# Kernel tuning notes

Measured on AMD Instinct MI355X. Metric: run time of the kernel, lower is better.

Reference implementation:

```python
import jax, jax.numpy as jnp
import numpy as np

B, T, F, H, O = 128, 4096, 80, 64, 8  # batch, seq_len, input_size, hidden_size, output_size


def setup_inputs() -> dict:
    key = jax.random.key(0)
    ks = jax.random.split(key, 12)
    s = 1.0 / np.sqrt(H)  # torch LSTM/Linear init scale

    def u(k, shape):
        return jax.random.uniform(k, shape, jnp.float32, -s, s)

    return {
        "x": jax.random.normal(ks[0], (B, T, F), jnp.float32),
        "lengths": jax.random.randint(ks[1], (B,), 1, T + 1),  # unused by forward, kept for signature fidelity
        "w_ih_f": u(ks[2], (4 * H, F)), "w_hh_f": u(ks[3], (4 * H, H)),
        "b_ih_f": u(ks[4], (4 * H,)), "b_hh_f": u(ks[5], (4 * H,)),
        "w_ih_b": u(ks[6], (4 * H, F)), "w_hh_b": u(ks[7], (4 * H, H)),
        "b_ih_b": u(ks[8], (4 * H,)), "b_hh_b": u(ks[9], (4 * H,)),
        "w_fc": u(ks[10], (O, 2 * H)), "b_fc": u(ks[11], (O,)),
    }


def _lstm_final_h(x, w_ih, w_hh, b_ih, b_hh):
    """Run a single-direction LSTM over x [B,T,F]; return final hidden state [B,H].
    PyTorch gate order: i, f, g, o."""
    pre = jnp.einsum('btf,gf->btg', x, w_ih) + (b_ih + b_hh)  # [B,T,4H], input projection hoisted out of scan
    h0 = jnp.zeros((x.shape[0], w_hh.shape[1]), x.dtype)

    def step(carry, g_t):
        h, c = carry
        gates = g_t + h @ w_hh.T  # [B,4H]
        i, f, g, o = jnp.split(gates, 4, axis=-1)
        c = jax.nn.sigmoid(f) * c + jax.nn.sigmoid(i) * jnp.tanh(g)
        h = jax.nn.sigmoid(o) * jnp.tanh(c)
        return (h, c), None

    (h, _), _ = jax.lax.scan(step, (h0, h0), jnp.swapaxes(pre, 0, 1))  # scan over time
    return h


def reference(x, lengths, w_ih_f, w_hh_f, b_ih_f, b_hh_f,
              w_ih_b, w_hh_b, b_ih_b, b_hh_b, w_fc, b_fc):
    # Bidirectional LSTM final hidden states: h[0]=forward final, h[1]=backward final.
    h_fwd = _lstm_final_h(x, w_ih_f, w_hh_f, b_ih_f, b_hh_f)
    h_bwd = _lstm_final_h(jnp.flip(x, axis=1), w_ih_b, w_hh_b, b_ih_b, b_hh_b)
    # permute (1,0,2) + reshape(B, 2H) of h [2,B,H] == concat along feature dim
    h = jnp.concatenate([h_fwd, h_bwd], axis=-1)  # [B, 2H]
    # nn.Dropout(0.5) in eval mode is identity (deterministic baseline)
    out = h @ w_fc.T + b_fc  # [B, O]
    return jnp.squeeze(out)
```

## Files before the change

kernel.cpp:

```cpp
#include <hip/hip_runtime.h>
#include <hip/hip_bf16.h>

#define TT 4096
#define FF 80
#define HH 64
#define NB 128
#define TB 256
#define CT 8
#define XPAD 104
#define LOG2E 1.44269504088896340736f

using short8  = __attribute__((ext_vector_type(8))) short;
using floatx4 = __attribute__((ext_vector_type(4))) float;

__device__ __forceinline__ float sigm(float x)  { return __builtin_amdgcn_rcpf(1.0f + __expf(-x)); }
__device__ __forceinline__ float tanh_f(float x){ return 1.0f - 2.0f * __builtin_amdgcn_rcpf(1.0f + __expf(2.0f * x)); }

__device__ __forceinline__ unsigned short f2bf(float f) {
    unsigned u = __builtin_bit_cast(unsigned, f);
    u += 0x7fffu + ((u >> 16) & 1u);
    return (unsigned short)(u >> 16);
}
__device__ __forceinline__ float bflo(unsigned u) { return __builtin_bit_cast(float, u << 16); }
__device__ __forceinline__ float bfhi(unsigned u) { return __builtin_bit_cast(float, u & 0xffff0000u); }
__device__ __forceinline__ unsigned packbf2(float a, float b) {
    return (unsigned)f2bf(a) | ((unsigned)f2bf(b) << 16);
}

__device__ __forceinline__ unsigned short cvt_bf16(float f) {
    unsigned r;
    asm("v_cvt_pk_bf16_f32 %0, %1, %2" : "=v"(r) : "v"(f), "v"(f));
    return (unsigned short)r;
}

__device__ __forceinline__ void bar_lgkm() {
    asm volatile("s_waitcnt lgkmcnt(0)" ::: "memory");
    __builtin_amdgcn_s_barrier();
}

__device__ __forceinline__ floatx4 mfma16(short8 a, short8 b, floatx4 c) {
    return __builtin_amdgcn_mfma_f32_16x16x32_bf16(a, b, c, 0, 0, 0);
}

__device__ __forceinline__ float sigm_s(float s) {
    return __builtin_amdgcn_rcpf(1.0f + __builtin_amdgcn_exp2f(-s));
}
__device__ __forceinline__ float tanh_s(float s) {
    return fmaf(-2.0f, __builtin_amdgcn_rcpf(1.0f + __builtin_amdgcn_exp2f(s + s)), 1.0f);
}

__global__ __launch_bounds__(256, 1)
void lstm_proj_mfma(const float* __restrict__ x,
                    const float* __restrict__ w_ih_f, const float* __restrict__ b_ih_f,
                    const float* __restrict__ b_hh_f,
                    const float* __restrict__ w_ih_b, const float* __restrict__ b_ih_b,
                    const float* __restrict__ b_hh_b,
                    unsigned short* __restrict__ pre)
{
    const int blk   = blockIdx.x;
    const int ttile = blk & 15;
    const int dgrp  = blk >> 4;
    const int dir   = dgrp >> 3;
    const int bgrp  = dgrp & 7;
    const int tid   = threadIdx.x;
    const int wv    = tid >> 6;
    const int l     = tid & 63;
    const int b16   = l & 15;
    const int g     = l >> 4;
    const int t0    = ttile * TB;

    const float* __restrict__ wih = dir ? w_ih_b : w_ih_f;
    const float* __restrict__ bi  = dir ? b_ih_b : b_ih_f;
    const float* __restrict__ bh  = dir ? b_hh_b : b_hh_f;

    short8 Bf[4][3];
    float  bias[4];
    #pragma unroll
    for (int tp = 0; tp < 4; ++tp) {
        const int n = 64 * wv + 16 * tp + b16;
        bias[tp] = (bi[n] + bh[n]) * LOG2E;
        #pragma unroll
        for (int kap = 0; kap < 3; ++kap) {
            const int f0 = 32 * kap + 8 * g;
            float f[8];
            if (f0 < FF) {
                const float4 v0 = *reinterpret_cast<const float4*>(wih + n * FF + f0);
                const float4 v1 = *reinterpret_cast<const float4*>(wih + n * FF + f0 + 4);
                f[0]=v0.x; f[1]=v0.y; f[2]=v0.z; f[3]=v0.w;
                f[4]=v1.x; f[5]=v1.y; f[6]=v1.z; f[7]=v1.w;
            } else {
                #pragma unroll
                for (int j = 0; j < 8; ++j) f[j] = 0.0f;
            }
            short8 s;
            #pragma unroll
            for (int j = 0; j < 8; ++j) s[j] = (short)f2bf(f[j] * LOG2E);
            Bf[tp][kap] = s;
        }
    }

    __shared__ __align__(16) unsigned short xa[2][CT][16][XPAD];
    for (int i = tid; i < 2 * CT * 16 * XPAD / 2; i += 256)
        reinterpret_cast<unsigned*>(&xa[0][0][0][0])[i] = 0u;
    __syncthreads();

    const int nph = TB / CT;

    {
        const int t0p = t0;
        const int te_base = dir ? (TT - CT - t0p) : t0p;
        float2 st[20];
        #pragma unroll
        for (int q = 0; q < 20; ++q) {
            const int i = q * 256 + tid;
            const int b = i / 320, r2 = i % 320;
            const int te_rel = r2 / 40, fq = r2 % 40;
            st[q] = *reinterpret_cast<const float2*>(
                x + ((size_t)(bgrp * 16 + b) * TT + te_base + te_rel) * FF + 2 * fq);
        }
        #pragma unroll
        for (int q = 0; q < 20; ++q) {
            const int i = q * 256 + tid;
            const int b = i / 320, r2 = i % 320;
            const int te_rel = r2 / 40, fq = r2 % 40;
            const int t_off = dir ? (CT - 1 - te_rel) : te_rel;
            *reinterpret_cast<unsigned*>(&xa[0][t_off][b][2 * fq]) = packbf2(st[q].x, st[q].y);
        }
    }
    __syncthreads();

    #pragma unroll 1
    for (int ph = 0; ph < nph; ++ph) {
        const int cur = ph & 1;
        const bool have = (ph + 1) < nph;

        float2 st[20];
        if (have) {
            const int t0p = t0 + (ph + 1) * CT;
            const int te_base = dir ? (TT - CT - t0p) : t0p;
            #pragma unroll
            for (int q = 0; q < 20; ++q) {
                const int i = q * 256 + tid;
                const int b = i / 320, r2 = i % 320;
                const int te_rel = r2 / 40, fq = r2 % 40;
                st[q] = *reinterpret_cast<const float2*>(
                    x + ((size_t)(bgrp * 16 + b) * TT + te_base + te_rel) * FF + 2 * fq);
            }
        }

        #pragma unroll
        for (int t_off = 0; t_off < CT; ++t_off) {
            short8 A[3];
            #pragma unroll
            for (int kap = 0; kap < 3; ++kap)
                A[kap] = *reinterpret_cast<const short8*>(&xa[cur][t_off][b16][32 * kap + 8 * g]);
            const int t = t0 + ph * CT + t_off;
            #pragma unroll
            for (int tp = 0; tp < 4; ++tp) {
                floatx4 acc = {bias[tp], bias[tp], bias[tp], bias[tp]};
                acc = mfma16(A[0], Bf[tp][0], acc);
                acc = mfma16(A[1], Bf[tp][1], acc);
                acc = mfma16(A[2], Bf[tp][2], acc);
                const int p = (16 * tp + b16) * 4 + wv;
                #pragma unroll
                for (int r = 0; r < 4; ++r) {
                    const int bb = dir * NB + bgrp * 16 + 4 * g + r;
                    pre[((size_t)bb * TT + t) * 256 + p] = f2bf(acc[r]);
                }
            }
        }

        if (have) {
            #pragma unroll
            for (int q = 0; q < 20; ++q) {
                const int i = q * 256 + tid;
                const int b = i / 320, r2 = i % 320;
                const int te_rel = r2 / 40, fq = r2 % 40;
                const int t_off = dir ? (CT - 1 - te_rel) : te_rel;
                *reinterpret_cast<unsigned*>(&xa[cur ^ 1][t_off][b][2 * fq]) = packbf2(st[q].x, st[q].y);
            }
        }
        bar_lgkm();
    }
}

__global__ __launch_bounds__(256, 1)
void lstm_scan_mfma4(const unsigned short* __restrict__ pre,
                     const float* __restrict__ w_hh_f, const float* __restrict__ w_hh_b,
                     float* __restrict__ h_out)
{
    const int chain = blockIdx.x;
    const int dir   = chain >> 7;
    const int tid   = threadIdx.x;
    const int wv    = tid >> 6;
    const int l     = tid & 63;
    const int b16   = l & 15;
    const int g4    = l >> 4;
    const bool actC = (g4 == 0);
    const int  u    = 16 * wv + b16;

    const float* __restrict__ whh = dir ? w_hh_b : w_hh_f;

    short8 Bf[4][2];
    #pragma unroll
    for (int gt = 0; gt < 4; ++gt) {
        const int n = gt * 64 + 16 * wv + b16;
        #pragma unroll
        for (int kap = 0; kap < 2; ++kap) {
            const float4 v0 = *reinterpret_cast<const float4*>(whh + n * HH + 32 * kap + 8 * g4);
            const float4 v1 = *reinterpret_cast<const float4*>(whh + n * HH + 32 * kap + 8 * g4 + 4);
            short8 s;
            s[0]=(short)f2bf(v0.x*LOG2E); s[1]=(short)f2bf(v0.y*LOG2E);
            s[2]=(short)f2bf(v0.z*LOG2E); s[3]=(short)f2bf(v0.w*LOG2E);
            s[4]=(short)f2bf(v1.x*LOG2E); s[5]=(short)f2bf(v1.y*LOG2E);
            s[6]=(short)f2bf(v1.z*LOG2E); s[7]=(short)f2bf(v1.w*LOG2E);
            Bf[gt][kap] = s;
        }
    }

    __shared__ __align__(16) unsigned short hls[192];
    if (tid < 96) reinterpret_cast<unsigned*>(hls)[tid] = 0u;

    const uint2* __restrict__ prow = reinterpret_cast<const uint2*>(
        pre + (size_t)chain * TT * 256 + u * 4);
    uint2 prr[4];
    if (actC) {
        #pragma unroll
        for (int d = 0; d < 4; ++d) prr[d] = prow[(size_t)d * 64];
    }

    float c = 0.0f, h = 0.0f;
    __syncthreads();

    const char* lb = reinterpret_cast<const char*>(hls);
    char* lw = reinterpret_cast<char*>(hls);

    #pragma unroll 1
    for (int t = 0; t < TT; t += 4) {
        #pragma unroll
        for (int d = 0; d < 4; ++d) {
            const int cur = d & 1;

            const int abase = (b16 == 0 ? 128 * cur : 256) + 16 * g4;
            const short8 A0 = *reinterpret_cast<const short8*>(lb + abase);
            const short8 A1 = *reinterpret_cast<const short8*>(lb + abase + 64);

            uint2 pc = prr[d];
            if (actC) prr[d] = prow[(size_t)((t + d + 4) & (TT - 1)) * 64];

            const floatx4 z = {0.f, 0.f, 0.f, 0.f};
            floatx4 ci0 = mfma16(A0, Bf[0][0], z), ci1 = mfma16(A1, Bf[0][1], z);
            floatx4 cf0 = mfma16(A0, Bf[1][0], z), cf1 = mfma16(A1, Bf[1][1], z);
            floatx4 cg0 = mfma16(A0, Bf[2][0], z), cg1 = mfma16(A1, Bf[2][1], z);
            floatx4 co0 = mfma16(A0, Bf[3][0], z), co1 = mfma16(A1, Bf[3][1], z);

            if (actC) {
                const float gi = bflo(pc.x) + (ci0[0] + ci1[0]);
                const float gf = bfhi(pc.x) + (cf0[0] + cf1[0]);
                const float gg = bflo(pc.y) + (cg0[0] + cg1[0]);
                const float go = bfhi(pc.y) + (co0[0] + co1[0]);
                c = fmaf(sigm_s(gf), c, sigm_s(gi) * tanh_s(gg));
                h = sigm_s(go) * tanh_s(c * LOG2E);
                *reinterpret_cast<unsigned short*>(lw + 128 * (cur ^ 1) + 2 * u) = cvt_bf16(h);
            }
            bar_lgkm();
        }
    }

    if (actC) h_out[(size_t)chain * HH + u] = h;
}

__global__ __launch_bounds__(256, 1)
void lstm_scan_fused_kernel(const float* __restrict__ x,
                            const float* __restrict__ w_ih_f, const float* __restrict__ w_hh_f,
                            const float* __restrict__ b_ih_f, const float* __restrict__ b_hh_f,
                            const float* __restrict__ w_ih_b, const float* __restrict__ w_hh_b,
                            const float* __restrict__ b_ih_b, const float* __restrict__ b_hh_b,
                            float* __restrict__ h_out)
{
    const int blk = blockIdx.x;
    const int dir = blk >> 7;
    const int bat = blk & 127;
    const int tid = threadIdx.x;
    const int wv  = tid >> 6;
    const int ln  = tid & 63;

    const float* __restrict__ w_ih = dir ? w_ih_b : w_ih_f;
    const float* __restrict__ w_hh = dir ? w_hh_b : w_hh_f;
    const float* __restrict__ b_ih = dir ? b_ih_b : b_ih_f;
    const float* __restrict__ b_hh = dir ? b_hh_b : b_hh_f;

    float wi[FF], wh[HH];
    #pragma unroll
    for (int f = 0; f < FF; ++f) wi[f] = w_ih[tid * FF + f];
    #pragma unroll
    for (int j = 0; j < HH; ++j) wh[j] = w_hh[tid * HH + j];
    const float bias = b_ih[tid] + b_hh[tid];

    __shared__ float xs[2][FF];
    __shared__ float hbuf[4][HH];
    __shared__ float gbuf[2][256];

    const float* __restrict__ xrow = x + (size_t)bat * (TT * FF);
    float c = 0.0f, hreg = 0.0f;
    hbuf[wv][ln] = 0.0f;

    float xA = 0.0f;
    if (tid < FF) {
        xs[0][tid] = xrow[(size_t)(dir ? (TT - 1) : 0) * FF + tid];
        xA         = xrow[(size_t)(dir ? (TT - 2) : 1) * FF + tid];
    }
    __syncthreads();

    #pragma unroll 1
    for (int t = 0; t < TT; ++t) {
        const int cur = t & 1, nxt = cur ^ 1;
        float a0 = 0.f, a1 = 0.f, a2 = 0.f, a3 = 0.f;
        const float4* xs4 = reinterpret_cast<const float4*>(xs[cur]);
        #pragma unroll
        for (int f = 0; f < FF / 4; ++f) {
            float4 v = xs4[f];
            a0 = fmaf(wi[4*f+0], v.x, a0);
            a1 = fmaf(wi[4*f+1], v.y, a1);
            a2 = fmaf(wi[4*f+2], v.z, a2);
            a3 = fmaf(wi[4*f+3], v.w, a3);
        }
        const float4* hb4 = reinterpret_cast<const float4*>(hbuf[wv]);
        #pragma unroll
        for (int j = 0; j < HH / 4; ++j) {
            float4 v = hb4[j];
            a0 = fmaf(wh[4*j+0], v.x, a0);
            a1 = fmaf(wh[4*j+1], v.y, a1);
            a2 = fmaf(wh[4*j+2], v.z, a2);
            a3 = fmaf(wh[4*j+3], v.w, a3);
        }
        gbuf[cur][tid] = ((a0 + a1) + (a2 + a3)) + bias;

        if (tid < FF) {
            if (t + 1 < TT) xs[nxt][tid] = xA;
            if (t + 2 < TT) xA = xrow[(size_t)(dir ? (TT - 3 - t) : (t + 2)) * FF + tid];
        }
        __syncthreads();

        const float gi = gbuf[cur][ln];
        const float gf = gbuf[cur][64 + ln];
        const float gg = gbuf[cur][128 + ln];
        const float go = gbuf[cur][192 + ln];
        c    = sigm(gf) * c + sigm(gi) * tanh_f(gg);
        hreg = sigm(go) * tanh_f(c);
        hbuf[wv][ln] = hreg;
    }

    if (tid < HH) h_out[(size_t)(dir * 128 + bat) * HH + tid] = hreg;
}

__global__ __launch_bounds__(64, 1)
void fc_kernel(const float* __restrict__ h_out,
               const float* __restrict__ w_fc,
               const float* __restrict__ b_fc,
               float* __restrict__ out)
{
    const int b = blockIdx.x;
    const int o = threadIdx.x;
    if (o < 8) {
        float acc = b_fc[o];
        #pragma unroll 4
        for (int j = 0; j < HH; ++j)
            acc = fmaf(h_out[(size_t)b * HH + j], w_fc[o * 128 + j], acc);
        #pragma unroll 4
        for (int j = 0; j < HH; ++j)
            acc = fmaf(h_out[(size_t)(NB + b) * HH + j], w_fc[o * 128 + 64 + j], acc);
        out[b * 8 + o] = acc;
    }
}

extern "C" void kernel_launch(void* const* d_in, const int* in_sizes, int n_in,
                              void* d_out, int out_size, void* d_ws, size_t ws_size,
                              hipStream_t stream) {
    const float* x      = (const float*)d_in[0];
    const float* w_ih_f = (const float*)d_in[2];
    const float* w_hh_f = (const float*)d_in[3];
    const float* b_ih_f = (const float*)d_in[4];
    const float* b_hh_f = (const float*)d_in[5];
    const float* w_ih_b = (const float*)d_in[6];
    const float* w_hh_b = (const float*)d_in[7];
    const float* b_ih_b = (const float*)d_in[8];
    const float* b_hh_b = (const float*)d_in[9];
    const float* w_fc   = (const float*)d_in[10];
    const float* b_fc   = (const float*)d_in[11];
    float* out = (float*)d_out;

    const size_t pre_bytes = (size_t)2 * NB * TT * 256 * 2;
    const size_t need      = pre_bytes + 64 * 1024;

    if (ws_size >= need) {
        unsigned short* pre = (unsigned short*)d_ws;
        float* h_out = (float*)((char*)d_ws + pre_bytes);
        lstm_proj_mfma<<<dim3(256), dim3(256), 0, stream>>>(
            x, w_ih_f, b_ih_f, b_hh_f, w_ih_b, b_ih_b, b_hh_b, pre);
        lstm_scan_mfma4<<<dim3(256), dim3(256), 0, stream>>>(
            pre, w_hh_f, w_hh_b, h_out);
        fc_kernel<<<dim3(128), dim3(64), 0, stream>>>(h_out, w_fc, b_fc, out);
    } else {
        float* h_out = (float*)d_ws;
        lstm_scan_fused_kernel<<<dim3(256), dim3(256), 0, stream>>>(
            x, w_ih_f, w_hh_f, b_ih_f, b_hh_f,
            w_ih_b, w_hh_b, b_ih_b, b_hh_b, h_out);
        fc_kernel<<<dim3(128), dim3(64), 0, stream>>>(h_out, w_fc, b_fc, out);
    }
}
```

Before: 1.431 ms.

## Interleave two LSTM chains per block in the recurrent scan kernel

```diff
diff --git a/kernel.cpp b/kernel.cpp
--- a/kernel.cpp
+++ b/kernel.cpp
@@ -9,6 +9,7 @@
 #define CT 8
 #define XPAD 104
 #define LOG2E 1.44269504088896340736f
+#define K2E   2.88539008177792681472f
 
 using short8  = __attribute__((ext_vector_type(8))) short;
 using floatx4 = __attribute__((ext_vector_type(4))) float;
@@ -185,19 +186,22 @@
 }
 
 __global__ __launch_bounds__(256, 1)
-void lstm_scan_mfma4(const unsigned short* __restrict__ pre,
-                     const float* __restrict__ w_hh_f, const float* __restrict__ w_hh_b,
-                     float* __restrict__ h_out)
+void lstm_scan_dual(const unsigned short* __restrict__ pre,
+                    const float* __restrict__ w_hh_f, const float* __restrict__ w_hh_b,
+                    float* __restrict__ h_out)
 {
-    const int chain = blockIdx.x;
-    const int dir   = chain >> 7;
-    const int tid   = threadIdx.x;
-    const int wv    = tid >> 6;
-    const int l     = tid & 63;
-    const int b16   = l & 15;
-    const int g4    = l >> 4;
-    const bool actC = (g4 == 0);
-    const int  u    = 16 * wv + b16;
+    const int blk    = blockIdx.x;
+    const int dir    = blk >> 6;
+    const int bat    = blk & 63;
+    const int chainA = dir * NB + bat;
+    const int chainB = chainA + 64;
+    const int tid    = threadIdx.x;
+    const int wv     = tid >> 6;
+    const int l      = tid & 63;
+    const int b16    = l & 15;
+    const int g4     = l >> 4;
+    const bool actC  = (g4 == 0);
+    const int  u     = 16 * wv + b16;
 
     const float* __restrict__ whh = dir ? w_hh_b : w_hh_f;
 
@@ -218,18 +222,24 @@
         }
     }
 
-    __shared__ __align__(16) unsigned short hls[192];
-    if (tid < 96) reinterpret_cast<unsigned*>(hls)[tid] = 0u;
-
-    const uint2* __restrict__ prow = reinterpret_cast<const uint2*>(
-        pre + (size_t)chain * TT * 256 + u * 4);
-    uint2 prr[4];
+    __shared__ __align__(16) unsigned short hls[320];
+    if (tid < 160) reinterpret_cast<unsigned*>(hls)[tid] = 0u;
+
+    const uint2* __restrict__ prowA = reinterpret_cast<const uint2*>(
+        pre + (size_t)chainA * TT * 256 + u * 4);
+    const uint2* __restrict__ prowB = reinterpret_cast<const uint2*>(
+        pre + (size_t)chainB * TT * 256 + u * 4);
+    uint2 prA[4] = {{0,0},{0,0},{0,0},{0,0}};
+    uint2 prB[4] = {{0,0},{0,0},{0,0},{0,0}};
+    const uint2 *pA0 = prowA + 4*64, *pA1 = prowA + 5*64, *pA2 = prowA + 6*64, *pA3 = prowA + 7*64;
+    const uint2 *pB0 = prowB + 4*64, *pB1 = prowB + 5*64, *pB2 = prowB + 6*64, *pB3 = prowB + 7*64;
     if (actC) {
-        #pragma unroll
-        for (int d = 0; d < 4; ++d) prr[d] = prow[(size_t)d * 64];
-    }
-
-    float c = 0.0f, h = 0.0f;
+        prA[0] = prowA[0*64]; prA[1] = prowA[1*64]; prA[2] = prowA[2*64]; prA[3] = prowA[3*64];
+        prB[0] = prowB[0*64]; prB[1] = prowB[1*64]; prB[2] = prowB[2*64]; prB[3] = prowB[3*64];
+    }
+
+    float c2A = 0.0f, hA = 0.0f;
+    float c2B = 0.0f, hB = 0.0f;
     __syncthreads();
 
     const char* lb = reinterpret_cast<const char*>(hls);
@@ -241,33 +251,67 @@
         for (int d = 0; d < 4; ++d) {
             const int cur = d & 1;
 
-            const int abase = (b16 == 0 ? 128 * cur : 256) + 16 * g4;
-            const short8 A0 = *reinterpret_cast<const short8*>(lb + abase);
-            const short8 A1 = *reinterpret_cast<const short8*>(lb + abase + 64);
-
-            uint2 pc = prr[d];
-            if (actC) prr[d] = prow[(size_t)((t + d + 4) & (TT - 1)) * 64];
+            const int abaseA = (b16 == 0 ? 128 * cur       : 256) + 16 * g4;
+            const int abaseB = (b16 == 0 ? 384 + 128 * cur : 256) + 16 * g4;
+            const short8 A0a = *reinterpret_cast<const short8*>(lb + abaseA);
+            const short8 A1a = *reinterpret_cast<const short8*>(lb + abaseA + 64);
+            const short8 A0b = *reinterpret_cast<const short8*>(lb + abaseB);
+            const short8 A1b = *reinterpret_cast<const short8*>(lb + abaseB + 64);
+
+            uint2 pcA = prA[d], pcB = prB[d];
+            if (actC) {
+                if (d == 0)      { prA[0] = *pA0; pA0 += 256; prB[0] = *pB0; pB0 += 256; }
+                else if (d == 1) { prA[1] = *pA1; pA1 += 256; prB[1] = *pB1; pB1 += 256; }
+                else if (d == 2) { prA[2] = *pA2; pA2 += 256; prB[2] = *pB2; pB2 += 256; }
+                else             { prA[3] = *pA3; pA3 += 256; prB[3] = *pB3; pB3 += 256; }
+            }
 
             const floatx4 z = {0.f, 0.f, 0.f, 0.f};
-            floatx4 ci0 = mfma16(A0, Bf[0][0], z), ci1 = mfma16(A1, Bf[0][1], z);
-            floatx4 cf0 = mfma16(A0, Bf[1][0], z), cf1 = mfma16(A1, Bf[1][1], z);
-            floatx4 cg0 = mfma16(A0, Bf[2][0], z), cg1 = mfma16(A1, Bf[2][1], z);
-            floatx4 co0 = mfma16(A0, Bf[3][0], z), co1 = mfma16(A1, Bf[3][1], z);
+            const floatx4 ciA = mfma16(A1a, Bf[0][1], mfma16(A0a, Bf[0][0], z));
+            const floatx4 ciB = mfma16(A1b, Bf[0][1], mfma16(A0b, Bf[0][0], z));
+            const floatx4 cfA = mfma16(A1a, Bf[1][1], mfma16(A0a, Bf[1][0], z));
+            const floatx4 cfB = mfma16(A1b, Bf[1][1], mfma16(A0b, Bf[1][0], z));
+            const floatx4 cgA = mfma16(A1a, Bf[2][1], mfma16(A0a, Bf[2][0], z));
+            const floatx4 cgB = mfma16(A1b, Bf[2][1], mfma16(A0b, Bf[2][0], z));
+            const floatx4 coA = mfma16(A1a, Bf[3][1], mfma16(A0a, Bf[3][0], z));
+            const floatx4 coB = mfma16(A1b, Bf[3][1], mfma16(A0b, Bf[3][0], z));
 
             if (actC) {
-                const float gi = bflo(pc.x) + (ci0[0] + ci1[0]);
-                const float gf = bfhi(pc.x) + (cf0[0] + cf1[0]);
-                const float gg = bflo(pc.y) + (cg0[0] + cg1[0]);
-                const float go = bfhi(pc.y) + (co0[0] + co1[0]);
-                c = fmaf(sigm_s(gf), c, sigm_s(gi) * tanh_s(gg));
-                h = sigm_s(go) * tanh_s(c * LOG2E);
-                *reinterpret_cast<unsigned short*>(lw + 128 * (cur ^ 1) + 2 * u) = cvt_bf16(h);
+                {
+                    const float gi = bflo(pcA.x) + ciA[0];
+                    const float gf = bfhi(pcA.x) + cfA[0];
+                    const float gg = bflo(pcA.y) + cgA[0];
+                    const float go = bfhi(pcA.y) + coA[0];
+                    const float si = sigm_s(gi), sf = sigm_s(gf);
+                    const float tg = tanh_s(gg), so = sigm_s(go);
+                    c2A = fmaf(sf, c2A, K2E * (si * tg));
+                    const float th = fmaf(-2.0f,
+                        __builtin_amdgcn_rcpf(1.0f + __builtin_amdgcn_exp2f(c2A)), 1.0f);
+                    hA = so * th;
+                    *reinterpret_cast<unsigned short*>(lw + 128 * (cur ^ 1) + 2 * u) = cvt_bf16(hA);
+                }
+                {
+                    const float gi = bflo(pcB.x) + ciB[0];
+                    const float gf = bfhi(pcB.x) + cfB[0];
+                    const float gg = bflo(pcB.y) + cgB[0];
+                    const float go = bfhi(pcB.y) + coB[0];
+                    const float si = sigm_s(gi), sf = sigm_s(gf);
+                    const float tg = tanh_s(gg), so = sigm_s(go);
+                    c2B = fmaf(sf, c2B, K2E * (si * tg));
+                    const float th = fmaf(-2.0f,
+                        __builtin_amdgcn_rcpf(1.0f + __builtin_amdgcn_exp2f(c2B)), 1.0f);
+                    hB = so * th;
+                    *reinterpret_cast<unsigned short*>(lw + 384 + 128 * (cur ^ 1) + 2 * u) = cvt_bf16(hB);
+                }
             }
             bar_lgkm();
         }
     }
 
-    if (actC) h_out[(size_t)chain * HH + u] = h;
+    if (actC) {
+        h_out[(size_t)chainA * HH + u] = hA;
+        h_out[(size_t)chainB * HH + u] = hB;
+    }
 }
 
 __global__ __launch_bounds__(256, 1)
@@ -398,7 +442,7 @@
         float* h_out = (float*)((char*)d_ws + pre_bytes);
         lstm_proj_mfma<<<dim3(256), dim3(256), 0, stream>>>(
             x, w_ih_f, b_ih_f, b_hh_f, w_ih_b, b_ih_b, b_hh_b, pre);
-        lstm_scan_mfma4<<<dim3(256), dim3(256), 0, stream>>>(
+        lstm_scan_dual<<<dim3(128), dim3(256), 0, stream>>>(
             pre, w_hh_f, w_hh_b, h_out);
         fc_kernel<<<dim3(128), dim3(64), 0, stream>>>(h_out, w_fc, b_fc, out);
     } else {
```

Measured after the change: 1.944 ms. 1.36x slower.

## Run recurrent LSTM scan in a single wave with 32x32 MFMA, no barriers

Applied to the files above, without the earlier changes.

```diff
diff --git a/kernel.cpp b/kernel.cpp
--- a/kernel.cpp
+++ b/kernel.cpp
@@ -9,9 +9,11 @@
 #define CT 8
 #define XPAD 104
 #define LOG2E 1.44269504088896340736f
-
-using short8  = __attribute__((ext_vector_type(8))) short;
-using floatx4 = __attribute__((ext_vector_type(4))) float;
+#define K2E   2.88539008177792681472f
+
+using short8   = __attribute__((ext_vector_type(8))) short;
+using floatx4  = __attribute__((ext_vector_type(4))) float;
+using floatx16 = __attribute__((ext_vector_type(16))) float;
 
 __device__ __forceinline__ float sigm(float x)  { return __builtin_amdgcn_rcpf(1.0f + __expf(-x)); }
 __device__ __forceinline__ float tanh_f(float x){ return 1.0f - 2.0f * __builtin_amdgcn_rcpf(1.0f + __expf(2.0f * x)); }
@@ -26,22 +28,21 @@
 __device__ __forceinline__ unsigned packbf2(float a, float b) {
     return (unsigned)f2bf(a) | ((unsigned)f2bf(b) << 16);
 }
-
 __device__ __forceinline__ unsigned short cvt_bf16(float f) {
     unsigned r;
     asm("v_cvt_pk_bf16_f32 %0, %1, %2" : "=v"(r) : "v"(f), "v"(f));
     return (unsigned short)r;
 }
-
 __device__ __forceinline__ void bar_lgkm() {
     asm volatile("s_waitcnt lgkmcnt(0)" ::: "memory");
     __builtin_amdgcn_s_barrier();
 }
-
 __device__ __forceinline__ floatx4 mfma16(short8 a, short8 b, floatx4 c) {
     return __builtin_amdgcn_mfma_f32_16x16x32_bf16(a, b, c, 0, 0, 0);
 }
-
+__device__ __forceinline__ floatx16 mfma32(short8 a, short8 b, floatx16 c) {
+    return __builtin_amdgcn_mfma_f32_32x32x16_bf16(a, b, c, 0, 0, 0);
+}
 __device__ __forceinline__ float sigm_s(float s) {
     return __builtin_amdgcn_rcpf(1.0f + __builtin_amdgcn_exp2f(-s));
 }
@@ -161,7 +162,8 @@
                 acc = mfma16(A[0], Bf[tp][0], acc);
                 acc = mfma16(A[1], Bf[tp][1], acc);
                 acc = mfma16(A[2], Bf[tp][2], acc);
-                const int p = (16 * tp + b16) * 4 + wv;
+                const int u_ = 16 * tp + b16;
+                const int p  = (u_ & 31) * 8 + (u_ >> 5) * 4 + wv;
                 #pragma unroll
                 for (int r = 0; r < 4; ++r) {
                     const int bb = dir * NB + bgrp * 16 + 4 * g + r;
@@ -184,53 +186,58 @@
     }
 }
 
-__global__ __launch_bounds__(256, 1)
-void lstm_scan_mfma4(const unsigned short* __restrict__ pre,
-                     const float* __restrict__ w_hh_f, const float* __restrict__ w_hh_b,
-                     float* __restrict__ h_out)
+__global__ __launch_bounds__(64, 1)
+void lstm_scan_solo(const unsigned short* __restrict__ pre,
+                    const float* __restrict__ w_hh_f, const float* __restrict__ w_hh_b,
+                    float* __restrict__ h_out)
 {
     const int chain = blockIdx.x;
     const int dir   = chain >> 7;
-    const int tid   = threadIdx.x;
-    const int wv    = tid >> 6;
-    const int l     = tid & 63;
-    const int b16   = l & 15;
-    const int g4    = l >> 4;
-    const bool actC = (g4 == 0);
-    const int  u    = 16 * wv + b16;
+    const int l     = threadIdx.x;
+    const int lh    = l >> 5;
+    const int lc    = l & 31;
+    const bool act  = (l < 32);
 
     const float* __restrict__ whh = dir ? w_hh_b : w_hh_f;
 
-    short8 Bf[4][2];
+    short8 B[8][4];
     #pragma unroll
-    for (int gt = 0; gt < 4; ++gt) {
-        const int n = gt * 64 + 16 * wv + b16;
-        #pragma unroll
-        for (int kap = 0; kap < 2; ++kap) {
-            const float4 v0 = *reinterpret_cast<const float4*>(whh + n * HH + 32 * kap + 8 * g4);
-            const float4 v1 = *reinterpret_cast<const float4*>(whh + n * HH + 32 * kap + 8 * g4 + 4);
+    for (int tau = 0; tau < 8; ++tau) {
+        const int n = (tau >> 1) * 64 + (tau & 1) * 32 + lc;
+        #pragma unroll
+        for (int kap = 0; kap < 4; ++kap) {
+            const float* src = whh + n * HH + 16 * kap + 8 * lh;
+            const float4 v0 = *reinterpret_cast<const float4*>(src);
+            const float4 v1 = *reinterpret_cast<const float4*>(src + 4);
             short8 s;
             s[0]=(short)f2bf(v0.x*LOG2E); s[1]=(short)f2bf(v0.y*LOG2E);
             s[2]=(short)f2bf(v0.z*LOG2E); s[3]=(short)f2bf(v0.w*LOG2E);
             s[4]=(short)f2bf(v1.x*LOG2E); s[5]=(short)f2bf(v1.y*LOG2E);
             s[6]=(short)f2bf(v1.z*LOG2E); s[7]=(short)f2bf(v1.w*LOG2E);
-            Bf[gt][kap] = s;
+            B[tau][kap] = s;
         }
     }
 
     __shared__ __align__(16) unsigned short hls[192];
-    if (tid < 96) reinterpret_cast<unsigned*>(hls)[tid] = 0u;
-
-    const uint2* __restrict__ prow = reinterpret_cast<const uint2*>(
-        pre + (size_t)chain * TT * 256 + u * 4);
-    uint2 prr[4];
-    if (actC) {
-        #pragma unroll
-        for (int d = 0; d < 4; ++d) prr[d] = prow[(size_t)d * 64];
-    }
-
-    float c = 0.0f, h = 0.0f;
+    for (int i = l; i < 96; i += 64)
+        reinterpret_cast<unsigned*>(hls)[i] = 0u;
     __syncthreads();
+
+    const int b0   = (lc == 0 ? 16 * lh : 256 + 16 * lh);
+    const int bAdd = (lc == 0 ? 128 : 0);
+
+    const uint4* __restrict__ prow =
+        reinterpret_cast<const uint4*>(pre + (size_t)chain * TT * 256) + lc;
+    uint4 pr[4] = {{0,0,0,0},{0,0,0,0},{0,0,0,0},{0,0,0,0}};
+    const uint4 *pp0 = prow + 4 * 32, *pp1 = prow + 5 * 32,
+                *pp2 = prow + 6 * 32, *pp3 = prow + 7 * 32;
+    if (act) {
+        pr[0] = prow[0 * 32]; pr[1] = prow[1 * 32];
+        pr[2] = prow[2 * 32]; pr[3] = prow[3 * 32];
+    }
+
+    float c2A = 0.0f, hA = 0.0f;
+    float c2B = 0.0f, hB = 0.0f;
 
     const char* lb = reinterpret_cast<const char*>(hls);
     char* lw = reinterpret_cast<char*>(hls);
@@ -241,33 +248,67 @@
         for (int d = 0; d < 4; ++d) {
             const int cur = d & 1;
 
-            const int abase = (b16 == 0 ? 128 * cur : 256) + 16 * g4;
-            const short8 A0 = *reinterpret_cast<const short8*>(lb + abase);
-            const short8 A1 = *reinterpret_cast<const short8*>(lb + abase + 64);
-
-            uint2 pc = prr[d];
-            if (actC) prr[d] = prow[(size_t)((t + d + 4) & (TT - 1)) * 64];
-
-            const floatx4 z = {0.f, 0.f, 0.f, 0.f};
-            floatx4 ci0 = mfma16(A0, Bf[0][0], z), ci1 = mfma16(A1, Bf[0][1], z);
-            floatx4 cf0 = mfma16(A0, Bf[1][0], z), cf1 = mfma16(A1, Bf[1][1], z);
-            floatx4 cg0 = mfma16(A0, Bf[2][0], z), cg1 = mfma16(A1, Bf[2][1], z);
-            floatx4 co0 = mfma16(A0, Bf[3][0], z), co1 = mfma16(A1, Bf[3][1], z);
-
-            if (actC) {
-                const float gi = bflo(pc.x) + (ci0[0] + ci1[0]);
-                const float gf = bfhi(pc.x) + (cf0[0] + cf1[0]);
-                const float gg = bflo(pc.y) + (cg0[0] + cg1[0]);
-                const float go = bfhi(pc.y) + (co0[0] + co1[0]);
-                c = fmaf(sigm_s(gf), c, sigm_s(gi) * tanh_s(gg));
-                h = sigm_s(go) * tanh_s(c * LOG2E);
-                *reinterpret_cast<unsigned short*>(lw + 128 * (cur ^ 1) + 2 * u) = cvt_bf16(h);
-            }
-            bar_lgkm();
-        }
-    }
-
-    if (actC) h_out[(size_t)chain * HH + u] = h;
+            const char* ab = lb + b0 + (cur ? bAdd : 0);
+            const short8 A0 = *reinterpret_cast<const short8*>(ab);
+            const short8 A1 = *reinterpret_cast<const short8*>(ab + 32);
+            const short8 A2 = *reinterpret_cast<const short8*>(ab + 64);
+            const short8 A3 = *reinterpret_cast<const short8*>(ab + 96);
+
+            const uint4 pc = pr[d];
+            if (act) {
+                if (d == 0)      { pr[0] = *pp0; pp0 += 128; }
+                else if (d == 1) { pr[1] = *pp1; pp1 += 128; }
+                else if (d == 2) { pr[2] = *pp2; pp2 += 128; }
+                else             { pr[3] = *pp3; pp3 += 128; }
+            }
+
+            const floatx16 z = {0.f,0.f,0.f,0.f,0.f,0.f,0.f,0.f,
+                                0.f,0.f,0.f,0.f,0.f,0.f,0.f,0.f};
+            const floatx16 a0 = mfma32(A3,B[0][3], mfma32(A2,B[0][2], mfma32(A1,B[0][1], mfma32(A0,B[0][0], z))));
+            const floatx16 a1 = mfma32(A3,B[1][3], mfma32(A2,B[1][2], mfma32(A1,B[1][1], mfma32(A0,B[1][0], z))));
+            const floatx16 a2 = mfma32(A3,B[2][3], mfma32(A2,B[2][2], mfma32(A1,B[2][1], mfma32(A0,B[2][0], z))));
+            const floatx16 a3 = mfma32(A3,B[3][3], mfma32(A2,B[3][2], mfma32(A1,B[3][1], mfma32(A0,B[3][0], z))));
+            const floatx16 a4 = mfma32(A3,B[4][3], mfma32(A2,B[4][2], mfma32(A1,B[4][1], mfma32(A0,B[4][0], z))));
+            const floatx16 a5 = mfma32(A3,B[5][3], mfma32(A2,B[5][2], mfma32(A1,B[5][1], mfma32(A0,B[5][0], z))));
+            const floatx16 a6 = mfma32(A3,B[6][3], mfma32(A2,B[6][2], mfma32(A1,B[6][1], mfma32(A0,B[6][0], z))));
+            const floatx16 a7 = mfma32(A3,B[7][3], mfma32(A2,B[7][2], mfma32(A1,B[7][1], mfma32(A0,B[7][0], z))));
+
+            if (act) {
+                const float giA = bflo(pc.x) + a0[0];
+                const float gfA = bfhi(pc.x) + a2[0];
+                const float ggA = bflo(pc.y) + a4[0];
+                const float goA = bfhi(pc.y) + a6[0];
+                const float giB = bflo(pc.z) + a1[0];
+                const float gfB = bfhi(pc.z) + a3[0];
+                const float ggB = bflo(pc.w) + a5[0];
+                const float goB = bfhi(pc.w) + a7[0];
+
+                {
+                    const float si = sigm_s(giA), sf = sigm_s(gfA);
+                    const float tg = tanh_s(ggA), so = sigm_s(goA);
+                    c2A = fmaf(sf, c2A, K2E * (si * tg));
+                    const float th = fmaf(-2.0f,
+                        __builtin_amdgcn_rcpf(1.0f + __builtin_amdgcn_exp2f(c2A)), 1.0f);
+                    hA = so * th;
+                }
+                {
+                    const float si = sigm_s(giB), sf = sigm_s(gfB);
+                    const float tg = tanh_s(ggB), so = sigm_s(goB);
+                    c2B = fmaf(sf, c2B, K2E * (si * tg));
+                    const float th = fmaf(-2.0f,
+                        __builtin_amdgcn_rcpf(1.0f + __builtin_amdgcn_exp2f(c2B)), 1.0f);
+                    hB = so * th;
+                }
+                *reinterpret_cast<unsigned short*>(lw + 128 * (cur ^ 1) + 2 * lc)      = cvt_bf16(hA);
+                *reinterpret_cast<unsigned short*>(lw + 128 * (cur ^ 1) + 64 + 2 * lc) = cvt_bf16(hB);
+            }
+        }
+    }
+
+    if (act) {
+        h_out[(size_t)chain * HH + lc]      = hA;
+        h_out[(size_t)chain * HH + 32 + lc] = hB;
+    }
 }
 
 __global__ __launch_bounds__(256, 1)
@@ -398,7 +439,7 @@
         float* h_out = (float*)((char*)d_ws + pre_bytes);
         lstm_proj_mfma<<<dim3(256), dim3(256), 0, stream>>>(
             x, w_ih_f, b_ih_f, b_hh_f, w_ih_b, b_ih_b, b_hh_b, pre);
-        lstm_scan_mfma4<<<dim3(256), dim3(256), 0, stream>>>(
+        lstm_scan_solo<<<dim3(256), dim3(64), 0, stream>>>(
             pre, w_hh_f, w_hh_b, h_out);
         fc_kernel<<<dim3(128), dim3(64), 0, stream>>>(h_out, w_fc, b_fc, out);
     } else {
```

New measurement: 3.873 ms. 171% more time.

## Halve scan block to two waves, each computing two hidden-unit tiles

Applied to the files above, without the earlier changes.

```diff
diff --git a/kernel.cpp b/kernel.cpp
--- a/kernel.cpp
+++ b/kernel.cpp
@@ -9,6 +9,7 @@
 #define CT 8
 #define XPAD 104
 #define LOG2E 1.44269504088896340736f
+#define K2E   2.88539008177792681472f
 
 using short8  = __attribute__((ext_vector_type(8))) short;
 using floatx4 = __attribute__((ext_vector_type(4))) float;
@@ -26,22 +27,18 @@
 __device__ __forceinline__ unsigned packbf2(float a, float b) {
     return (unsigned)f2bf(a) | ((unsigned)f2bf(b) << 16);
 }
-
 __device__ __forceinline__ unsigned short cvt_bf16(float f) {
     unsigned r;
     asm("v_cvt_pk_bf16_f32 %0, %1, %2" : "=v"(r) : "v"(f), "v"(f));
     return (unsigned short)r;
 }
-
 __device__ __forceinline__ void bar_lgkm() {
     asm volatile("s_waitcnt lgkmcnt(0)" ::: "memory");
     __builtin_amdgcn_s_barrier();
 }
-
 __device__ __forceinline__ floatx4 mfma16(short8 a, short8 b, floatx4 c) {
     return __builtin_amdgcn_mfma_f32_16x16x32_bf16(a, b, c, 0, 0, 0);
 }
-
 __device__ __forceinline__ float sigm_s(float s) {
     return __builtin_amdgcn_rcpf(1.0f + __builtin_amdgcn_exp2f(-s));
 }
@@ -184,10 +181,10 @@
     }
 }
 
-__global__ __launch_bounds__(256, 1)
-void lstm_scan_mfma4(const unsigned short* __restrict__ pre,
-                     const float* __restrict__ w_hh_f, const float* __restrict__ w_hh_b,
-                     float* __restrict__ h_out)
+__global__ __launch_bounds__(128, 1)
+void lstm_scan_w2(const unsigned short* __restrict__ pre,
+                  const float* __restrict__ w_hh_f, const float* __restrict__ w_hh_b,
+                  float* __restrict__ h_out)
 {
     const int chain = blockIdx.x;
     const int dir   = chain >> 7;
@@ -197,39 +194,49 @@
     const int b16   = l & 15;
     const int g4    = l >> 4;
     const bool actC = (g4 == 0);
-    const int  u    = 16 * wv + b16;
+    const int  u0   = 32 * wv + b16;
+    const int  u1   = u0 + 16;
 
     const float* __restrict__ whh = dir ? w_hh_b : w_hh_f;
 
-    short8 Bf[4][2];
+    short8 Bf[4][2][2];
     #pragma unroll
     for (int gt = 0; gt < 4; ++gt) {
-        const int n = gt * 64 + 16 * wv + b16;
-        #pragma unroll
-        for (int kap = 0; kap < 2; ++kap) {
-            const float4 v0 = *reinterpret_cast<const float4*>(whh + n * HH + 32 * kap + 8 * g4);
-            const float4 v1 = *reinterpret_cast<const float4*>(whh + n * HH + 32 * kap + 8 * g4 + 4);
-            short8 s;
-            s[0]=(short)f2bf(v0.x*LOG2E); s[1]=(short)f2bf(v0.y*LOG2E);
-            s[2]=(short)f2bf(v0.z*LOG2E); s[3]=(short)f2bf(v0.w*LOG2E);
-            s[4]=(short)f2bf(v1.x*LOG2E); s[5]=(short)f2bf(v1.y*LOG2E);
-            s[6]=(short)f2bf(v1.z*LOG2E); s[7]=(short)f2bf(v1.w*LOG2E);
-            Bf[gt][kap] = s;
+        #pragma unroll
+        for (int tp = 0; tp < 2; ++tp) {
+            const int n = gt * 64 + 32 * wv + 16 * tp + b16;
+            #pragma unroll
+            for (int kap = 0; kap < 2; ++kap) {
+                const float4 v0 = *reinterpret_cast<const float4*>(whh + n * HH + 32 * kap + 8 * g4);
+                const float4 v1 = *reinterpret_cast<const float4*>(whh + n * HH + 32 * kap + 8 * g4 + 4);
+                short8 s;
+                s[0]=(short)f2bf(v0.x*LOG2E); s[1]=(short)f2bf(v0.y*LOG2E);
+                s[2]=(short)f2bf(v0.z*LOG2E); s[3]=(short)f2bf(v0.w*LOG2E);
+                s[4]=(short)f2bf(v1.x*LOG2E); s[5]=(short)f2bf(v1.y*LOG2E);
+                s[6]=(short)f2bf(v1.z*LOG2E); s[7]=(short)f2bf(v1.w*LOG2E);
+                Bf[gt][tp][kap] = s;
+            }
         }
     }
 
     __shared__ __align__(16) unsigned short hls[192];
     if (tid < 96) reinterpret_cast<unsigned*>(hls)[tid] = 0u;
 
-    const uint2* __restrict__ prow = reinterpret_cast<const uint2*>(
-        pre + (size_t)chain * TT * 256 + u * 4);
-    uint2 prr[4];
+    const uint2* __restrict__ prow0 = reinterpret_cast<const uint2*>(
+        pre + (size_t)chain * TT * 256 + u0 * 4);
+    const uint2* __restrict__ prow1 = reinterpret_cast<const uint2*>(
+        pre + (size_t)chain * TT * 256 + u1 * 4);
+    uint2 prA[4] = {{0,0},{0,0},{0,0},{0,0}};
+    uint2 prB[4] = {{0,0},{0,0},{0,0},{0,0}};
+    const uint2 *pA0 = prow0 + 4*64, *pA1 = prow0 + 5*64, *pA2 = prow0 + 6*64, *pA3 = prow0 + 7*64;
+    const uint2 *pB0 = prow1 + 4*64, *pB1 = prow1 + 5*64, *pB2 = prow1 + 6*64, *pB3 = prow1 + 7*64;
     if (actC) {
-        #pragma unroll
-        for (int d = 0; d < 4; ++d) prr[d] = prow[(size_t)d * 64];
-    }
-
-    float c = 0.0f, h = 0.0f;
+        prA[0] = prow0[0*64]; prA[1] = prow0[1*64]; prA[2] = prow0[2*64]; prA[3] = prow0[3*64];
+        prB[0] = prow1[0*64]; prB[1] = prow1[1*64]; prB[2] = prow1[2*64]; prB[3] = prow1[3*64];
+    }
+
+    float c2A = 0.0f, hA = 0.0f;
+    float c2B = 0.0f, hB = 0.0f;
     __syncthreads();
 
     const char* lb = reinterpret_cast<const char*>(hls);
@@ -245,29 +252,60 @@
             const short8 A0 = *reinterpret_cast<const short8*>(lb + abase);
             const short8 A1 = *reinterpret_cast<const short8*>(lb + abase + 64);
 
-            uint2 pc = prr[d];
-            if (actC) prr[d] = prow[(size_t)((t + d + 4) & (TT - 1)) * 64];
+            uint2 pcA = prA[d], pcB = prB[d];
+            if (actC) {
+                if (d == 0)      { prA[0] = *pA0; pA0 += 256; prB[0] = *pB0; pB0 += 256; }
+                else if (d == 1) { prA[1] = *pA1; pA1 += 256; prB[1] = *pB1; pB1 += 256; }
+                else if (d == 2) { prA[2] = *pA2; pA2 += 256; prB[2] = *pB2; pB2 += 256; }
+                else             { prA[3] = *pA3; pA3 += 256; prB[3] = *pB3; pB3 += 256; }
+            }
 
             const floatx4 z = {0.f, 0.f, 0.f, 0.f};
-            floatx4 ci0 = mfma16(A0, Bf[0][0], z), ci1 = mfma16(A1, Bf[0][1], z);
-            floatx4 cf0 = mfma16(A0, Bf[1][0], z), cf1 = mfma16(A1, Bf[1][1], z);
-            floatx4 cg0 = mfma16(A0, Bf[2][0], z), cg1 = mfma16(A1, Bf[2][1], z);
-            floatx4 co0 = mfma16(A0, Bf[3][0], z), co1 = mfma16(A1, Bf[3][1], z);
+            const floatx4 ci0 = mfma16(A1, Bf[0][0][1], mfma16(A0, Bf[0][0][0], z));
+            const floatx4 ci1 = mfma16(A1, Bf[0][1][1], mfma16(A0, Bf[0][1][0], z));
+            const floatx4 cf0 = mfma16(A1, Bf[1][0][1], mfma16(A0, Bf[1][0][0], z));
+            const floatx4 cf1 = mfma16(A1, Bf[1][1][1], mfma16(A0, Bf[1][1][0], z));
+            const floatx4 cg0 = mfma16(A1, Bf[2][0][1], mfma16(A0, Bf[2][0][0], z));
+            const floatx4 cg1 = mfma16(A1, Bf[2][1][1], mfma16(A0, Bf[2][1][0], z));
+            const floatx4 co0 = mfma16(A1, Bf[3][0][1], mfma16(A0, Bf[3][0][0], z));
+            const floatx4 co1 = mfma16(A1, Bf[3][1][1], mfma16(A0, Bf[3][1][0], z));
 
             if (actC) {
-                const float gi = bflo(pc.x) + (ci0[0] + ci1[0]);
-                const float gf = bfhi(pc.x) + (cf0[0] + cf1[0]);
-                const float gg = bflo(pc.y) + (cg0[0] + cg1[0]);
-                const float go = bfhi(pc.y) + (co0[0] + co1[0]);
-                c = fmaf(sigm_s(gf), c, sigm_s(gi) * tanh_s(gg));
-                h = sigm_s(go) * tanh_s(c * LOG2E);
-                *reinterpret_cast<unsigned short*>(lw + 128 * (cur ^ 1) + 2 * u) = cvt_bf16(h);
+                {
+                    const float gi = bflo(pcA.x) + ci0[0];
+                    const float gf = bfhi(pcA.x) + cf0[0];
+                    const float gg = bflo(pcA.y) + cg0[0];
+                    const float go = bfhi(pcA.y) + co0[0];
+                    const float si = sigm_s(gi), sf = sigm_s(gf);
+                    const float tg = tanh_s(gg), so = sigm_s(go);
+                    c2A = fmaf(sf, c2A, K2E * (si * tg));
+                    const float th = fmaf(-2.0f,
+                        __builtin_amdgcn_rcpf(1.0f + __builtin_amdgcn_exp2f(c2A)), 1.0f);
+                    hA = so * th;
+                }
+                {
+                    const float gi = bflo(pcB.x) + ci1[0];
+                    const float gf = bfhi(pcB.x) + cf1[0];
+                    const float gg = bflo(pcB.y) + cg1[0];
+                    const float go = bfhi(pcB.y) + co1[0];
+                    const float si = sigm_s(gi), sf = sigm_s(gf);
+                    const float tg = tanh_s(gg), so = sigm_s(go);
+                    c2B = fmaf(sf, c2B, K2E * (si * tg));
+                    const float th = fmaf(-2.0f,
+                        __builtin_amdgcn_rcpf(1.0f + __builtin_amdgcn_exp2f(c2B)), 1.0f);
+                    hB = so * th;
+                }
+                *reinterpret_cast<unsigned short*>(lw + 128 * (cur ^ 1) + 2 * u0) = cvt_bf16(hA);
+                *reinterpret_cast<unsigned short*>(lw + 128 * (cur ^ 1) + 2 * u1) = cvt_bf16(hB);
             }
             bar_lgkm();
         }
     }
 
-    if (actC) h_out[(size_t)chain * HH + u] = h;
+    if (actC) {
+        h_out[(size_t)chain * HH + u0] = hA;
+        h_out[(size_t)chain * HH + u1] = hB;
+    }
 }
 
 __global__ __launch_bounds__(256, 1)
@@ -398,7 +436,7 @@
         float* h_out = (float*)((char*)d_ws + pre_bytes);
         lstm_proj_mfma<<<dim3(256), dim3(256), 0, stream>>>(
             x, w_ih_f, b_ih_f, b_hh_f, w_ih_b, b_ih_b, b_hh_b, pre);
-        lstm_scan_mfma4<<<dim3(256), dim3(256), 0, stream>>>(
+        lstm_scan_w2<<<dim3(256), dim3(128), 0, stream>>>(
             pre, w_hh_f, w_hh_b, h_out);
         fc_kernel<<<dim3(128), dim3(64), 0, stream>>>(h_out, w_fc, b_fc, out);
     } else {
```

New measurement: 1.817 ms. +27.0%, slower.
